# Kernel optimization log

Hardware: AMD Instinct MI355X
Metric: run time of the kernel (lower is better)

Reference implementation:

```python
import math
import jax, jax.numpy as jnp
import numpy as np

N = 65536
S = 4            # n_scales
F = 64           # n_fourier
H = 256          # hidden
NB = 2           # res-blocks per branch (n_blocks=8 // n_scales=4)
IN_F = 2 + 8 * F # 514 fourier features per branch
OUT_DIM = 1
FREQ_MIN, FREQ_MAX = 1.0, 64.0


def setup_inputs() -> dict:
    key = jax.random.key(0)
    ks = jax.random.split(key, 10)
    xy = jax.random.uniform(ks[0], (N, 2), dtype=jnp.float32)
    # per-branch log-frequency init: linspace(log f_lo, log f_hi, F) within each scale band
    log_bounds = np.linspace(math.log(FREQ_MIN), math.log(FREQ_MAX), S + 1)
    w = np.stack([np.linspace(log_bounds[i], log_bounds[i + 1], F) for i in range(S)]).astype(np.float32)
    w_x = jnp.asarray(w)
    w_y = jnp.asarray(w)
    # NTK-parameterized linears: weight ~ N(0,1), bias = 0, scaled by 1/sqrt(fan_in) in forward
    proj_W = jax.random.normal(ks[1], (S, H, IN_F), dtype=jnp.float32)
    proj_b = jnp.zeros((S, H), dtype=jnp.float32)
    blk_W1 = jax.random.normal(ks[2], (S, NB, H, H), dtype=jnp.float32)
    blk_b1 = jnp.zeros((S, NB, H), dtype=jnp.float32)
    blk_W2 = jax.random.normal(ks[3], (S, NB, H, H), dtype=jnp.float32)
    blk_b2 = jnp.zeros((S, NB, H), dtype=jnp.float32)
    # head / shortcut are plain nn.Linear: use fan-in-scaled init baked into weights
    head_W = jax.random.normal(ks[4], (OUT_DIM, H), dtype=jnp.float32) / math.sqrt(H)
    head_b = jnp.zeros((OUT_DIM,), dtype=jnp.float32)
    sc_W = jax.random.normal(ks[5], (OUT_DIM, S * IN_F), dtype=jnp.float32) / math.sqrt(S * IN_F)
    return {"xy": xy, "w_x": w_x, "w_y": w_y, "proj_W": proj_W, "proj_b": proj_b,
            "blk_W1": blk_W1, "blk_b1": blk_b1, "blk_W2": blk_W2, "blk_b2": blk_b2,
            "head_W": head_W, "head_b": head_b, "sc_W": sc_W}


def _fourier(xy, w_x, w_y):
    # xy: [N,2]; w_x,w_y: [S,F] -> f: [S,N,2+8F]
    Bx = jnp.exp(w_x)[:, None, :]             # [S,1,F]
    By = jnp.exp(w_y)[:, None, :]
    px = jnp.pi * xy[None, :, 0:1] * Bx       # [S,N,F]
    py = jnp.pi * xy[None, :, 1:2] * By
    xy_b = jnp.broadcast_to(xy[None], (w_x.shape[0], xy.shape[0], 2))
    return jnp.concatenate([xy_b,
                            jnp.sin(px), jnp.cos(px),
                            jnp.sin(py), jnp.cos(py),
                            jnp.sin(px + py), jnp.cos(px + py),
                            jnp.sin(px - py), jnp.cos(px - py)], axis=-1)


def reference(xy, w_x, w_y, proj_W, proj_b, blk_W1, blk_b1, blk_W2, blk_b2, head_W, head_b, sc_W):
    gelu = lambda t: jax.nn.gelu(t, approximate=False)  # torch nn.GELU default = exact erf
    s_in = 1.0 / math.sqrt(IN_F)   # NTK scale for proj
    s_h = 1.0 / math.sqrt(H)       # NTK scale for block linears
    f = _fourier(xy, w_x, w_y)                                   # [S,N,IN_F]
    h = gelu(jnp.einsum('snf,shf->snh', f, proj_W) * s_in + proj_b[:, None, :])
    for b in range(NB):  # small fixed layer count
        t = gelu(jnp.einsum('snh,sgh->sng', h, blk_W1[:, b]) * s_h + blk_b1[:, b, None, :])
        h = h + jnp.einsum('sng,shg->snh', t, blk_W2[:, b]) * s_h + blk_b2[:, b, None, :]
    combined = jnp.sum(h, axis=0)                                # [N,H]
    out = combined @ head_W.T + head_b                           # [N,OUT_DIM]
    all_f = jnp.moveaxis(f, 0, 1).reshape(xy.shape[0], -1)       # [N, S*IN_F]
    return out + all_f @ sc_W.T
```

## Files before the change

### kernel.cpp

```cpp
#include <hip/hip_runtime.h>
#include <hip/hip_bf16.h>
#include <cmath>


#define NSC   4
#define NFREQ 64
#define HID   256
#define NBLK  2
#define INF   514
#define TM    64
#define NTHR  512

#define T_OFF    32768
#define SMEM_BYTES 65536

#define TILE_E   8192
#define PROJ_OFF(s)    ((s) * 131072)
#define W1_OFF   524288
#define W2_OFF   1048576
#define WSB_ELEMS 1572864

static constexpr float S_IN = 0.04411042041035620f;
static constexpr float S_H  = 0.0625f;
static constexpr float LOG2E = 1.4426950408889634f;

typedef __attribute__((ext_vector_type(8))) short bf16x8;
typedef __attribute__((ext_vector_type(4))) float f32x4;

__device__ __forceinline__ unsigned short f2bf(float v) {
  __hip_bfloat16 b = __float2bfloat16(v);
  unsigned short u;
  __builtin_memcpy(&u, &b, 2);
  return u;
}

__device__ __forceinline__ unsigned pack2(float a, float b) {
  return (unsigned)f2bf(a) | ((unsigned)f2bf(b) << 16);
}

__device__ __forceinline__ float geluf(float x) {
  const float z = fabsf(x) * 0.7071067811865476f;
  const float t = __builtin_amdgcn_rcpf(fmaf(0.3275911f, z, 1.0f));
  float p = 1.061405429f;
  p = fmaf(p, t, -1.453152027f);
  p = fmaf(p, t, 1.421413741f);
  p = fmaf(p, t, -0.284496736f);
  p = fmaf(p, t, 0.254829592f);
  const float e = __builtin_amdgcn_exp2f(-z * z * LOG2E);
  const float erf_ = 1.0f - p * t * e;
  return 0.5f * x * (1.0f + copysignf(erf_, x));
}

template<bool WS, bool PERM, int KSTEPS, int ROWB>
__device__ __forceinline__ void gemmK(const char* a_base,
                                      const unsigned short* __restrict__ wt,
                                      const float* __restrict__ wf,
                                      const int fp_rs, const int fp_co,
                                      const int lane, const int hq,
                                      f32x4 acc[2][4]) {
  const int ar = lane & 15;
  const int q  = lane >> 4;
  bf16x8 wb[2][2];

  auto loadw = [&](int ks, bf16x8 w[2]) {
#pragma unroll
    for (int hf = 0; hf < 2; ++hf) {
      const int row = hq * 32 + hf * 16 + ar;
      if constexpr (WS) {
        w[hf] = *(const bf16x8*)(wt + ks * TILE_E + row * 32 + q * 8);
      } else if constexpr (PERM) {
        const int j = ks * 4 + q;
        const float* p = wf + row * fp_rs + fp_co;
#pragma unroll
        for (int e = 0; e < 8; ++e) w[hf][e] = (short)f2bf(p[e * 64 + j]);
      } else {
        const float* p = wf + row * fp_rs + fp_co + ks * 32 + q * 8;
#pragma unroll
        for (int e = 0; e < 8; ++e) w[hf][e] = (short)f2bf(p[e]);
      }
    }
  };

  loadw(0, wb[0]);
#pragma unroll
  for (int ks = 0; ks < KSTEPS; ++ks) {
    if (ks + 1 < KSTEPS) loadw(ks + 1, wb[(ks + 1) & 1]);
    __builtin_amdgcn_s_setprio(1);
#pragma unroll
    for (int pf = 0; pf < 4; ++pf) {
      const int pt = pf * 16 + ar;
      const int slot = (ks * 4 + q) ^ (pt & 7);
      const bf16x8 a = *(const bf16x8*)(a_base + pt * ROWB + (slot << 4));
      acc[0][pf] = __builtin_amdgcn_mfma_f32_16x16x32_bf16(wb[ks & 1][0], a,
                                                           acc[0][pf], 0, 0, 0);
      acc[1][pf] = __builtin_amdgcn_mfma_f32_16x16x32_bf16(wb[ks & 1][1], a,
                                                           acc[1][pf], 0, 0, 0);
    }
    __builtin_amdgcn_s_setprio(0);
  }
}

__global__ void cvt_weights(const float* __restrict__ projW,
                            const float* __restrict__ w1,
                            const float* __restrict__ w2,
                            unsigned short* __restrict__ o) {
  const int tot = WSB_ELEMS;
  for (int i = blockIdx.x * blockDim.x + threadIdx.x; i < tot;
       i += gridDim.x * blockDim.x) {
    float v;
    if (i < W1_OFF) {
      const int s = i >> 17, r = i & 131071;
      const int kst = r >> 13, rr = r & 8191;
      const int h = rr >> 5, kw = rr & 31;
      const int kp = kst * 32 + kw;
      const int j = kp >> 3, g = kp & 7;
      v = projW[(s * HID + h) * INF + 2 + g * 64 + j];
    } else if (i < W2_OFF) {
      const int i2 = i - W1_OFF;
      const int w = i2 >> 16, r = i2 & 65535;
      const int kst = r >> 13, h = (r >> 5) & 255, kw = r & 31;
      v = w1[w * 65536 + h * HID + kst * 32 + kw];
    } else {
      const int i2 = i - W2_OFF;
      const int w = i2 >> 16, r = i2 & 65535;
      const int kst = r >> 13, h = (r >> 5) & 255, kw = r & 31;
      v = w2[w * 65536 + h * HID + kst * 32 + kw];
    }
    o[i] = f2bf(v);
  }
}

template<bool WS>
__global__ __launch_bounds__(NTHR, 4)
void fnet_fused(const float* __restrict__ xy,
                const float* __restrict__ w_x,
                const float* __restrict__ w_y,
                const float* __restrict__ proj_W,
                const float* __restrict__ proj_b,
                const float* __restrict__ blk_W1,
                const float* __restrict__ blk_b1,
                const float* __restrict__ blk_W2,
                const float* __restrict__ blk_b2,
                const float* __restrict__ head_W,
                const float* __restrict__ head_b,
                const float* __restrict__ sc_W,
                const unsigned short* __restrict__ wsb,
                float* __restrict__ out) {
  extern __shared__ char smem[];
  char* f_arena = smem;
  char* h_base  = smem;
  char* t_base  = smem + T_OFF;

  const int tid  = threadIdx.x;
  const int lane = tid & 63;
  const int wave = tid >> 6;
  const int hq   = wave;
  const int m0   = blockIdx.x * TM;
  const int ar   = lane & 15;
  const int q    = lane >> 4;
  const float hb0 = head_b[0];

  auto tile_addr = [&](char* base, int hf, int pf) -> char* {
    const int pt = pf * 16 + ar;
    const int slot = (hq * 4 + hf * 2 + (q >> 1)) ^ (pt & 7);
    return base + pt * 512 + (slot << 4) + (q & 1) * 8;
  };

  f32x4 acc[2][4];
  auto zacc = [&]() {
#pragma unroll
    for (int a_ = 0; a_ < 2; ++a_)
#pragma unroll
      for (int b_ = 0; b_ < 4; ++b_) acc[a_][b_] = (f32x4)0.f;
  };

  for (int s = 0; s < NSC; ++s) {
    __syncthreads();

    {
      const int fj = lane;
      const float bx = __builtin_amdgcn_exp2f(w_x[s * NFREQ + fj] * LOG2E);
      const float by = __builtin_amdgcn_exp2f(w_y[s * NFREQ + fj] * LOG2E);
      float sc8[8];
#pragma unroll
      for (int g2 = 0; g2 < 8; ++g2) sc8[g2] = sc_W[s * INF + 2 + g2 * NFREQ + fj];
      const float scW0 = sc_W[s * INF], scW1 = sc_W[s * INF + 1];
#pragma unroll 2
      for (int p = 0; p < 8; ++p) {
        const int pt = wave * 8 + p;
        const float x  = xy[(m0 + pt) * 2];
        const float yv = xy[(m0 + pt) * 2 + 1];
        float tx = 0.5f * x * bx;  tx -= floorf(tx);
        float ty = 0.5f * yv * by; ty -= floorf(ty);
        const float sx = __builtin_amdgcn_sinf(tx);
        const float cx = __builtin_amdgcn_cosf(tx);
        const float sy = __builtin_amdgcn_sinf(ty);
        const float cy = __builtin_amdgcn_cosf(ty);
        const float p1 = sx * cy, p2 = cx * sy, p3 = cx * cy, p4 = sx * sy;
        const float g0 = sx, g1 = cx, g2 = sy, g3 = cy;
        const float g4 = p1 + p2, g5 = p3 - p4, g6 = p1 - p2, g7 = p3 + p4;
        uint4 wv;
        wv.x = pack2(g0, g1); wv.y = pack2(g2, g3);
        wv.z = pack2(g4, g5); wv.w = pack2(g6, g7);
        *(uint4*)(f_arena + pt * 1024 + ((fj ^ (pt & 7)) << 4)) = wv;
        float psum = g0 * sc8[0] + g1 * sc8[1] + g2 * sc8[2] + g3 * sc8[3]
                   + g4 * sc8[4] + g5 * sc8[5] + g6 * sc8[6] + g7 * sc8[7];
        psum += __shfl_xor(psum, 1, 64);
        psum += __shfl_xor(psum, 2, 64);
        psum += __shfl_xor(psum, 4, 64);
        psum += __shfl_xor(psum, 8, 64);
        psum += __shfl_xor(psum, 16, 64);
        psum += __shfl_xor(psum, 32, 64);
        if (lane == 0)
          atomicAdd(&out[m0 + pt],
                    psum + x * scW0 + yv * scW1 + (s == 0 ? hb0 : 0.f));
      }
    }
    __syncthreads();

    zacc();
    gemmK<WS, true, 16, 1024>(f_arena, wsb + PROJ_OFF(s),
                              proj_W + s * HID * INF, INF, 2,
                              lane, hq, acc);
    __syncthreads();

#pragma unroll
    for (int hf = 0; hf < 2; ++hf) {
      const int Hb = hq * 32 + hf * 16 + 4 * q;
      const float4 pb4 = *(const float4*)(proj_b + s * HID + Hb);
      const float pbv[4] = {pb4.x, pb4.y, pb4.z, pb4.w};
      float wx0[4], wy0[4];
#pragma unroll
      for (int r = 0; r < 4; ++r) {
        const float2 w01 = *(const float2*)(proj_W + (size_t)(s * HID + Hb + r) * INF);
        wx0[r] = w01.x; wy0[r] = w01.y;
      }
#pragma unroll
      for (int pf = 0; pf < 4; ++pf) {
        const int pt = pf * 16 + ar;
        const float2 xp2 = *(const float2*)(xy + (m0 + pt) * 2);
        float hv[4];
#pragma unroll
        for (int r = 0; r < 4; ++r)
          hv[r] = geluf((acc[hf][pf][r] + xp2.x * wx0[r] + xp2.y * wy0[r]) * S_IN + pbv[r]);
        *(uint2*)tile_addr(h_base, hf, pf) =
            make_uint2(pack2(hv[0], hv[1]), pack2(hv[2], hv[3]));
      }
    }
    __syncthreads();

    for (int b = 0; b < NBLK; ++b) {
      const int wb_ = s * NBLK + b;
      zacc();
      gemmK<WS, false, 8, 512>(h_base, wsb + W1_OFF + wb_ * 65536,
                               blk_W1 + wb_ * 65536, HID, 0,
                               lane, hq, acc);
#pragma unroll
      for (int hf = 0; hf < 2; ++hf) {
        const int Hb = hq * 32 + hf * 16 + 4 * q;
        const float4 b14 = *(const float4*)(blk_b1 + wb_ * HID + Hb);
        const float b1v[4] = {b14.x, b14.y, b14.z, b14.w};
#pragma unroll
        for (int pf = 0; pf < 4; ++pf)
          *(uint2*)tile_addr(t_base, hf, pf) =
              make_uint2(pack2(geluf(acc[hf][pf][0] * S_H + b1v[0]),
                               geluf(acc[hf][pf][1] * S_H + b1v[1])),
                         pack2(geluf(acc[hf][pf][2] * S_H + b1v[2]),
                               geluf(acc[hf][pf][3] * S_H + b1v[3])));
      }
      __syncthreads();

      zacc();
      gemmK<WS, false, 8, 512>(t_base, wsb + W2_OFF + wb_ * 65536,
                               blk_W2 + wb_ * 65536, HID, 0,
                               lane, hq, acc);

      if (b + 1 < NBLK) {
#pragma unroll
        for (int hf = 0; hf < 2; ++hf) {
          const int Hb = hq * 32 + hf * 16 + 4 * q;
          const float4 b24 = *(const float4*)(blk_b2 + wb_ * HID + Hb);
          const float b2v[4] = {b24.x, b24.y, b24.z, b24.w};
#pragma unroll
          for (int pf = 0; pf < 4; ++pf) {
            const uint2 u = *(const uint2*)tile_addr(h_base, hf, pf);
            float hv[4];
            hv[0] = __uint_as_float(u.x << 16)         + acc[hf][pf][0] * S_H + b2v[0];
            hv[1] = __uint_as_float(u.x & 0xffff0000u) + acc[hf][pf][1] * S_H + b2v[1];
            hv[2] = __uint_as_float(u.y << 16)         + acc[hf][pf][2] * S_H + b2v[2];
            hv[3] = __uint_as_float(u.y & 0xffff0000u) + acc[hf][pf][3] * S_H + b2v[3];
            *(uint2*)tile_addr(h_base, hf, pf) =
                make_uint2(pack2(hv[0], hv[1]), pack2(hv[2], hv[3]));
          }
        }
      } else {
        float v[4] = {0.f, 0.f, 0.f, 0.f};
#pragma unroll
        for (int hf = 0; hf < 2; ++hf) {
          const int Hb = hq * 32 + hf * 16 + 4 * q;
          const float4 b24 = *(const float4*)(blk_b2 + wb_ * HID + Hb);
          const float4 hw4 = *(const float4*)(head_W + Hb);
#pragma unroll
          for (int pf = 0; pf < 4; ++pf) {
            const uint2 u = *(const uint2*)tile_addr(h_base, hf, pf);
            v[pf] += (__uint_as_float(u.x << 16)         + acc[hf][pf][0] * S_H + b24.x) * hw4.x
                   + (__uint_as_float(u.x & 0xffff0000u) + acc[hf][pf][1] * S_H + b24.y) * hw4.y
                   + (__uint_as_float(u.y << 16)         + acc[hf][pf][2] * S_H + b24.z) * hw4.z
                   + (__uint_as_float(u.y & 0xffff0000u) + acc[hf][pf][3] * S_H + b24.w) * hw4.w;
          }
        }
#pragma unroll
        for (int pf = 0; pf < 4; ++pf) {
          float vv = v[pf];
          vv += __shfl_xor(vv, 16, 64);
          vv += __shfl_xor(vv, 32, 64);
          if (lane < 16) atomicAdd(&out[m0 + pf * 16 + ar], vv);
        }
      }
      __syncthreads();
    }
  }
}

extern "C" void kernel_launch(void* const* d_in, const int* in_sizes, int n_in,
                              void* d_out, int out_size, void* d_ws, size_t ws_size,
                              hipStream_t stream) {
  (void)in_sizes; (void)n_in;
  const float* xy     = (const float*)d_in[0];
  const float* w_x    = (const float*)d_in[1];
  const float* w_y    = (const float*)d_in[2];
  const float* proj_W = (const float*)d_in[3];
  const float* proj_b = (const float*)d_in[4];
  const float* blk_W1 = (const float*)d_in[5];
  const float* blk_b1 = (const float*)d_in[6];
  const float* blk_W2 = (const float*)d_in[7];
  const float* blk_b2 = (const float*)d_in[8];
  const float* head_W = (const float*)d_in[9];
  const float* head_b = (const float*)d_in[10];
  const float* sc_W   = (const float*)d_in[11];
  float* out = (float*)d_out;

  const bool use_ws = ws_size >= (size_t)WSB_ELEMS * 2;
  const int nblocks = out_size / TM;

  (void)hipMemsetAsync(d_out, 0, (size_t)out_size * sizeof(float), stream);

  if (use_ws) {
    cvt_weights<<<768, 256, 0, stream>>>(proj_W, blk_W1, blk_W2,
                                         (unsigned short*)d_ws);
    fnet_fused<true><<<nblocks, NTHR, SMEM_BYTES, stream>>>(
        xy, w_x, w_y, proj_W, proj_b, blk_W1, blk_b1, blk_W2, blk_b2,
        head_W, head_b, sc_W, (const unsigned short*)d_ws, out);
  } else {
    fnet_fused<false><<<nblocks, NTHR, SMEM_BYTES, stream>>>(
        xy, w_x, w_y, proj_W, proj_b, blk_W1, blk_b1, blk_W2, blk_b2,
        head_W, head_b, sc_W, (const unsigned short*)nullptr, out);
  }
}
```

Measured before the change: 330.1 us.

## Switch MFMA tiles from 16x16x32 to 32x32x16 and re-lay out weights

Replaces the 16x16x32 bf16 MFMA path with 32x32x16 instructions, where each wave computes a 32-row by 64-point tile with two f32x16 accumulators. The pre-converted weight layout, the A-tile swizzle and all epilogue indexing are rewritten to match. This is meant to cut A-operand LDS reads and per-MFMA issue overhead per FLOP. It also removes the barrier at the top of each scale loop, which may race if the previous epilogue's final barrier does not cover it.

```diff
diff --git a/kernel.cpp b/kernel.cpp
--- a/kernel.cpp
+++ b/kernel.cpp
@@ -14,7 +14,7 @@
 #define T_OFF    32768
 #define SMEM_BYTES 65536
 
-#define TILE_E   8192
+#define TILE_E   4096
 #define PROJ_OFF(s)    ((s) * 131072)
 #define W1_OFF   524288
 #define W2_OFF   1048576
@@ -24,8 +24,8 @@
 static constexpr float S_H  = 0.0625f;
 static constexpr float LOG2E = 1.4426950408889634f;
 
-typedef __attribute__((ext_vector_type(8))) short bf16x8;
-typedef __attribute__((ext_vector_type(4))) float f32x4;
+typedef __attribute__((ext_vector_type(8)))  short bf16x8;
+typedef __attribute__((ext_vector_type(16))) float f32x16;
 
 __device__ __forceinline__ unsigned short f2bf(float v) {
   __hip_bfloat16 b = __float2bfloat16(v);
@@ -51,50 +51,49 @@
   return 0.5f * x * (1.0f + copysignf(erf_, x));
 }
 
-template<bool WS, bool PERM, int KSTEPS, int ROWB>
-__device__ __forceinline__ void gemmK(const char* a_base,
-                                      const unsigned short* __restrict__ wt,
-                                      const float* __restrict__ wf,
-                                      const int fp_rs, const int fp_co,
-                                      const int lane, const int hq,
-                                      f32x4 acc[2][4]) {
-  const int ar = lane & 15;
-  const int q  = lane >> 4;
-  bf16x8 wb[2][2];
-
-  auto loadw = [&](int ks, bf16x8 w[2]) {
-#pragma unroll
-    for (int hf = 0; hf < 2; ++hf) {
-      const int row = hq * 32 + hf * 16 + ar;
-      if constexpr (WS) {
-        w[hf] = *(const bf16x8*)(wt + ks * TILE_E + row * 32 + q * 8);
-      } else if constexpr (PERM) {
-        const int j = ks * 4 + q;
-        const float* p = wf + row * fp_rs + fp_co;
-#pragma unroll
-        for (int e = 0; e < 8; ++e) w[hf][e] = (short)f2bf(p[e * 64 + j]);
-      } else {
-        const float* p = wf + row * fp_rs + fp_co + ks * 32 + q * 8;
-#pragma unroll
-        for (int e = 0; e < 8; ++e) w[hf][e] = (short)f2bf(p[e]);
-      }
+template<bool WS, bool PERM, int KS16, int ROWB>
+__device__ __forceinline__ void gemm32(const char* a_base,
+                                       const unsigned short* __restrict__ wt,
+                                       const float* __restrict__ wf,
+                                       const int fp_rs, const int fp_co,
+                                       const int lane, const int hq,
+                                       f32x16 acc[2]) {
+  const int lr = lane & 31;
+  const int kg = lane >> 5;
+  bf16x8 wb[2];
+
+  auto loadw = [&](int ks) -> bf16x8 {
+    const int row = hq * 32 + lr;
+    if constexpr (WS) {
+      return *(const bf16x8*)(wt + ks * TILE_E + row * 16 + kg * 8);
+    } else if constexpr (PERM) {
+      const int j = ks * 2 + kg;
+      const float* p = wf + row * fp_rs + fp_co;
+      bf16x8 w;
+#pragma unroll
+      for (int e = 0; e < 8; ++e) w[e] = (short)f2bf(p[e * 64 + j]);
+      return w;
+    } else {
+      const float* p = wf + row * fp_rs + fp_co + ks * 16 + kg * 8;
+      bf16x8 w;
+#pragma unroll
+      for (int e = 0; e < 8; ++e) w[e] = (short)f2bf(p[e]);
+      return w;
     }
   };
 
-  loadw(0, wb[0]);
-#pragma unroll
-  for (int ks = 0; ks < KSTEPS; ++ks) {
-    if (ks + 1 < KSTEPS) loadw(ks + 1, wb[(ks + 1) & 1]);
+  wb[0] = loadw(0);
+#pragma unroll
+  for (int ks = 0; ks < KS16; ++ks) {
+    if (ks + 1 < KS16) wb[(ks + 1) & 1] = loadw(ks + 1);
+    const bf16x8 w = wb[ks & 1];
     __builtin_amdgcn_s_setprio(1);
 #pragma unroll
-    for (int pf = 0; pf < 4; ++pf) {
-      const int pt = pf * 16 + ar;
-      const int slot = (ks * 4 + q) ^ (pt & 7);
+    for (int pb = 0; pb < 2; ++pb) {
+      const int pt = pb * 32 + lr;
+      const int slot = (ks * 2 + kg) ^ (pt & 7);
       const bf16x8 a = *(const bf16x8*)(a_base + pt * ROWB + (slot << 4));
-      acc[0][pf] = __builtin_amdgcn_mfma_f32_16x16x32_bf16(wb[ks & 1][0], a,
-                                                           acc[0][pf], 0, 0, 0);
-      acc[1][pf] = __builtin_amdgcn_mfma_f32_16x16x32_bf16(wb[ks & 1][1], a,
-                                                           acc[1][pf], 0, 0, 0);
+      acc[pb] = __builtin_amdgcn_mfma_f32_32x32x16_bf16(w, a, acc[pb], 0, 0, 0);
     }
     __builtin_amdgcn_s_setprio(0);
   }
@@ -110,21 +109,21 @@
     float v;
     if (i < W1_OFF) {
       const int s = i >> 17, r = i & 131071;
-      const int kst = r >> 13, rr = r & 8191;
-      const int h = rr >> 5, kw = rr & 31;
-      const int kp = kst * 32 + kw;
+      const int kst = r >> 12, rr = r & 4095;
+      const int h = rr >> 4, kw = rr & 15;
+      const int kp = kst * 16 + kw;
       const int j = kp >> 3, g = kp & 7;
       v = projW[(s * HID + h) * INF + 2 + g * 64 + j];
     } else if (i < W2_OFF) {
       const int i2 = i - W1_OFF;
       const int w = i2 >> 16, r = i2 & 65535;
-      const int kst = r >> 13, h = (r >> 5) & 255, kw = r & 31;
-      v = w1[w * 65536 + h * HID + kst * 32 + kw];
+      const int kst = r >> 12, h = (r >> 4) & 255, kw = r & 15;
+      v = w1[w * 65536 + h * HID + kst * 16 + kw];
     } else {
       const int i2 = i - W2_OFF;
       const int w = i2 >> 16, r = i2 & 65535;
-      const int kst = r >> 13, h = (r >> 5) & 255, kw = r & 31;
-      v = w2[w * 65536 + h * HID + kst * 32 + kw];
+      const int kst = r >> 12, h = (r >> 4) & 255, kw = r & 15;
+      v = w2[w * 65536 + h * HID + kst * 16 + kw];
     }
     o[i] = f2bf(v);
   }
@@ -156,27 +155,23 @@
   const int wave = tid >> 6;
   const int hq   = wave;
   const int m0   = blockIdx.x * TM;
-  const int ar   = lane & 15;
-  const int q    = lane >> 4;
+  const int lr   = lane & 31;
+  const int kg   = lane >> 5;
   const float hb0 = head_b[0];
 
-  auto tile_addr = [&](char* base, int hf, int pf) -> char* {
-    const int pt = pf * 16 + ar;
-    const int slot = (hq * 4 + hf * 2 + (q >> 1)) ^ (pt & 7);
-    return base + pt * 512 + (slot << 4) + (q & 1) * 8;
+  auto tile_addr = [&](char* base, int pb, int grp) -> char* {
+    const int pt = pb * 32 + lr;
+    const int slot = (hq * 4 + grp) ^ (pt & 7);
+    return base + pt * 512 + (slot << 4) + kg * 8;
   };
 
-  f32x4 acc[2][4];
+  f32x16 acc[2];
   auto zacc = [&]() {
-#pragma unroll
-    for (int a_ = 0; a_ < 2; ++a_)
-#pragma unroll
-      for (int b_ = 0; b_ < 4; ++b_) acc[a_][b_] = (f32x4)0.f;
+    acc[0] = (f32x16)0.f;
+    acc[1] = (f32x16)0.f;
   };
 
   for (int s = 0; s < NSC; ++s) {
-    __syncthreads();
-
     {
       const int fj = lane;
       const float bx = __builtin_amdgcn_exp2f(w_x[s * NFREQ + fj] * LOG2E);
@@ -219,14 +214,14 @@
     __syncthreads();
 
     zacc();
-    gemmK<WS, true, 16, 1024>(f_arena, wsb + PROJ_OFF(s),
-                              proj_W + s * HID * INF, INF, 2,
-                              lane, hq, acc);
+    gemm32<WS, true, 32, 1024>(f_arena, wsb + PROJ_OFF(s),
+                               proj_W + s * HID * INF, INF, 2,
+                               lane, hq, acc);
     __syncthreads();
 
 #pragma unroll
-    for (int hf = 0; hf < 2; ++hf) {
-      const int Hb = hq * 32 + hf * 16 + 4 * q;
+    for (int grp = 0; grp < 4; ++grp) {
+      const int Hb = hq * 32 + grp * 8 + 4 * kg;
       const float4 pb4 = *(const float4*)(proj_b + s * HID + Hb);
       const float pbv[4] = {pb4.x, pb4.y, pb4.z, pb4.w};
       float wx0[4], wy0[4];
@@ -236,14 +231,15 @@
         wx0[r] = w01.x; wy0[r] = w01.y;
       }
 #pragma unroll
-      for (int pf = 0; pf < 4; ++pf) {
-        const int pt = pf * 16 + ar;
+      for (int pb = 0; pb < 2; ++pb) {
+        const int pt = pb * 32 + lr;
         const float2 xp2 = *(const float2*)(xy + (m0 + pt) * 2);
         float hv[4];
 #pragma unroll
         for (int r = 0; r < 4; ++r)
-          hv[r] = geluf((acc[hf][pf][r] + xp2.x * wx0[r] + xp2.y * wy0[r]) * S_IN + pbv[r]);
-        *(uint2*)tile_addr(h_base, hf, pf) =
+          hv[r] = geluf((acc[pb][grp * 4 + r] + xp2.x * wx0[r] + xp2.y * wy0[r])
+                            * S_IN + pbv[r]);
+        *(uint2*)tile_addr(h_base, pb, grp) =
             make_uint2(pack2(hv[0], hv[1]), pack2(hv[2], hv[3]));
       }
     }
@@ -252,69 +248,68 @@
     for (int b = 0; b < NBLK; ++b) {
       const int wb_ = s * NBLK + b;
       zacc();
-      gemmK<WS, false, 8, 512>(h_base, wsb + W1_OFF + wb_ * 65536,
-                               blk_W1 + wb_ * 65536, HID, 0,
-                               lane, hq, acc);
-#pragma unroll
-      for (int hf = 0; hf < 2; ++hf) {
-        const int Hb = hq * 32 + hf * 16 + 4 * q;
+      gemm32<WS, false, 16, 512>(h_base, wsb + W1_OFF + wb_ * 65536,
+                                 blk_W1 + wb_ * 65536, HID, 0,
+                                 lane, hq, acc);
+#pragma unroll
+      for (int grp = 0; grp < 4; ++grp) {
+        const int Hb = hq * 32 + grp * 8 + 4 * kg;
         const float4 b14 = *(const float4*)(blk_b1 + wb_ * HID + Hb);
         const float b1v[4] = {b14.x, b14.y, b14.z, b14.w};
 #pragma unroll
-        for (int pf = 0; pf < 4; ++pf)
-          *(uint2*)tile_addr(t_base, hf, pf) =
-              make_uint2(pack2(geluf(acc[hf][pf][0] * S_H + b1v[0]),
-                               geluf(acc[hf][pf][1] * S_H + b1v[1])),
-                         pack2(geluf(acc[hf][pf][2] * S_H + b1v[2]),
-                               geluf(acc[hf][pf][3] * S_H + b1v[3])));
+        for (int pb = 0; pb < 2; ++pb)
+          *(uint2*)tile_addr(t_base, pb, grp) =
+              make_uint2(pack2(geluf(acc[pb][grp * 4 + 0] * S_H + b1v[0]),
+                               geluf(acc[pb][grp * 4 + 1] * S_H + b1v[1])),
+                         pack2(geluf(acc[pb][grp * 4 + 2] * S_H + b1v[2]),
+                               geluf(acc[pb][grp * 4 + 3] * S_H + b1v[3])));
       }
       __syncthreads();
 
       zacc();
-      gemmK<WS, false, 8, 512>(t_base, wsb + W2_OFF + wb_ * 65536,
-                               blk_W2 + wb_ * 65536, HID, 0,
-                               lane, hq, acc);
+      gemm32<WS, false, 16, 512>(t_base, wsb + W2_OFF + wb_ * 65536,
+                                 blk_W2 + wb_ * 65536, HID, 0,
+                                 lane, hq, acc);
 
       if (b + 1 < NBLK) {
 #pragma unroll
-        for (int hf = 0; hf < 2; ++hf) {
-          const int Hb = hq * 32 + hf * 16 + 4 * q;
+        for (int grp = 0; grp < 4; ++grp) {
+          const int Hb = hq * 32 + grp * 8 + 4 * kg;
           const float4 b24 = *(const float4*)(blk_b2 + wb_ * HID + Hb);
           const float b2v[4] = {b24.x, b24.y, b24.z, b24.w};
 #pragma unroll
-          for (int pf = 0; pf < 4; ++pf) {
-            const uint2 u = *(const uint2*)tile_addr(h_base, hf, pf);
+          for (int pb = 0; pb < 2; ++pb) {
+            const uint2 u = *(const uint2*)tile_addr(h_base, pb, grp);
             float hv[4];
-            hv[0] = __uint_as_float(u.x << 16)         + acc[hf][pf][0] * S_H + b2v[0];
-            hv[1] = __uint_as_float(u.x & 0xffff0000u) + acc[hf][pf][1] * S_H + b2v[1];
-            hv[2] = __uint_as_float(u.y << 16)         + acc[hf][pf][2] * S_H + b2v[2];
-            hv[3] = __uint_as_float(u.y & 0xffff0000u) + acc[hf][pf][3] * S_H + b2v[3];
-            *(uint2*)tile_addr(h_base, hf, pf) =
+            hv[0] = __uint_as_float(u.x << 16)         + acc[pb][grp * 4 + 0] * S_H + b2v[0];
+            hv[1] = __uint_as_float(u.x & 0xffff0000u) + acc[pb][grp * 4 + 1] * S_H + b2v[1];
+            hv[2] = __uint_as_float(u.y << 16)         + acc[pb][grp * 4 + 2] * S_H + b2v[2];
+            hv[3] = __uint_as_float(u.y & 0xffff0000u) + acc[pb][grp * 4 + 3] * S_H + b2v[3];
+            *(uint2*)tile_addr(h_base, pb, grp) =
                 make_uint2(pack2(hv[0], hv[1]), pack2(hv[2], hv[3]));
           }
         }
       } else {
-        float v[4] = {0.f, 0.f, 0.f, 0.f};
-#pragma unroll
-        for (int hf = 0; hf < 2; ++hf) {
-          const int Hb = hq * 32 + hf * 16 + 4 * q;
+        float v[2] = {0.f, 0.f};
+#pragma unroll
+        for (int grp = 0; grp < 4; ++grp) {
+          const int Hb = hq * 32 + grp * 8 + 4 * kg;
           const float4 b24 = *(const float4*)(blk_b2 + wb_ * HID + Hb);
           const float4 hw4 = *(const float4*)(head_W + Hb);
 #pragma unroll
-          for (int pf = 0; pf < 4; ++pf) {
-            const uint2 u = *(const uint2*)tile_addr(h_base, hf, pf);
-            v[pf] += (__uint_as_float(u.x << 16)         + acc[hf][pf][0] * S_H + b24.x) * hw4.x
-                   + (__uint_as_float(u.x & 0xffff0000u) + acc[hf][pf][1] * S_H + b24.y) * hw4.y
-                   + (__uint_as_float(u.y << 16)         + acc[hf][pf][2] * S_H + b24.z) * hw4.z
-                   + (__uint_as_float(u.y & 0xffff0000u) + acc[hf][pf][3] * S_H + b24.w) * hw4.w;
+          for (int pb = 0; pb < 2; ++pb) {
+            const uint2 u = *(const uint2*)tile_addr(h_base, pb, grp);
+            v[pb] += (__uint_as_float(u.x << 16)         + acc[pb][grp * 4 + 0] * S_H + b24.x) * hw4.x
+                   + (__uint_as_float(u.x & 0xffff0000u) + acc[pb][grp * 4 + 1] * S_H + b24.y) * hw4.y
+                   + (__uint_as_float(u.y << 16)         + acc[pb][grp * 4 + 2] * S_H + b24.z) * hw4.z
+                   + (__uint_as_float(u.y & 0xffff0000u) + acc[pb][grp * 4 + 3] * S_H + b24.w) * hw4.w;
           }
         }
 #pragma unroll
-        for (int pf = 0; pf < 4; ++pf) {
-          float vv = v[pf];
-          vv += __shfl_xor(vv, 16, 64);
+        for (int pb = 0; pb < 2; ++pb) {
+          float vv = v[pb];
           vv += __shfl_xor(vv, 32, 64);
-          if (lane < 16) atomicAdd(&out[m0 + pf * 16 + ar], vv);
+          if (lane < 32) atomicAdd(&out[m0 + pb * 32 + lr], vv);
         }
       }
       __syncthreads();
```

New measurement: 399.4 us. +21.0%, slower.
